# Kernel tuning notes

Measured on AMD Instinct MI355X. Metric: run time of the kernel, lower is better.

Reference implementation:

```python
import jax, jax.numpy as jnp
import numpy as np

N_NODES = 50000
N_EDGES = 500000
N_GRAPHS = 512


def _segmean(vals, ids, num):
    # avg aggregation: segment mean with safe divide for empty segments
    s = jax.ops.segment_sum(vals, ids, num_segments=num)
    c = jax.ops.segment_sum(jnp.ones((vals.shape[0], 1), vals.dtype), ids, num_segments=num)
    return s / jnp.maximum(c, 1.0)


def setup_inputs() -> dict:
    key = jax.random.key(0)
    ks = iter(jax.random.split(key, 64))

    def nrm(shape, scale=0.05):
        return jax.random.normal(next(ks), shape, dtype=jnp.float32) * scale

    inp = {}
    inp['x'] = nrm((N_NODES, 64), 1.0)
    inp['e'] = nrm((N_EDGES, 32), 1.0)
    inp['u'] = nrm((N_GRAPHS, 64), 1.0)
    inp['a'] = nrm((N_GRAPHS, 8), 1.0)
    inp['senders'] = jax.random.randint(next(ks), (N_EDGES,), 0, N_NODES)
    inp['receivers'] = jax.random.randint(next(ks), (N_EDGES,), 0, N_NODES)
    inp['node_graph'] = jnp.sort(jax.random.randint(next(ks), (N_NODES,), 0, N_GRAPHS))
    inp['edge_graph'] = jnp.sort(jax.random.randint(next(ks), (N_EDGES,), 0, N_GRAPHS))
    # block 1 (hidden 256)
    inp['We1'] = nrm((32, 256)); inp['be1'] = jnp.zeros((256,), jnp.float32)
    inp['Wn1'] = nrm((64, 256)); inp['Win1'] = nrm((256, 256)); inp['Wout1'] = nrm((256, 256)); inp['bn1'] = jnp.zeros((256,), jnp.float32)
    inp['Wg1'] = nrm((64, 256)); inp['Wgn1'] = nrm((256, 256)); inp['Wge1'] = nrm((256, 256)); inp['bg1'] = jnp.zeros((256,), jnp.float32)
    # block 2 (hidden 128)
    inp['We2'] = nrm((256, 128)); inp['be2'] = jnp.zeros((128,), jnp.float32)
    inp['Wn2'] = nrm((256, 128)); inp['Win2'] = nrm((128, 128)); inp['Wout2'] = nrm((128, 128)); inp['bn2'] = jnp.zeros((128,), jnp.float32)
    inp['Wg2'] = nrm((256, 128)); inp['Wgn2'] = nrm((128, 128)); inp['Wge2'] = nrm((128, 128)); inp['bg2'] = jnp.zeros((128,), jnp.float32)
    # global readout (global_features only)
    inp['Wga'] = nrm((128, 128)); inp['bga'] = jnp.zeros((128,), jnp.float32)
    # action-value MLP: (128 + 8) -> 256 -> 256 -> 1
    inp['Wa1'] = nrm((136, 256)); inp['ba1'] = jnp.zeros((256,), jnp.float32)
    inp['Wa2'] = nrm((256, 256)); inp['ba2'] = jnp.zeros((256,), jnp.float32)
    inp['Wa3'] = nrm((256, 1)); inp['ba3'] = jnp.zeros((1,), jnp.float32)
    return inp


def reference(x, e, u, a, senders, receivers, node_graph, edge_graph,
              We1, be1, Wn1, Win1, Wout1, bn1, Wg1, Wgn1, Wge1, bg1,
              We2, be2, Wn2, Win2, Wout2, bn2, Wg2, Wgn2, Wge2, bg2,
              Wga, bga, Wa1, ba1, Wa2, ba2, Wa3, ba3):
    # --- GraphNetwork block 1 (hidden 256) ---
    e1 = jax.nn.relu(e @ We1 + be1)                                  # [E,256]
    inc1 = _segmean(e1, receivers, N_NODES)                          # avg incoming per node
    out1 = _segmean(e1, senders, N_NODES)                            # avg outgoing per node
    n1 = jax.nn.relu(x @ Wn1 + inc1 @ Win1 + out1 @ Wout1 + bn1)     # [N,256]
    u1 = jax.nn.relu(u @ Wg1 + _segmean(n1, node_graph, N_GRAPHS) @ Wgn1
                     + _segmean(e1, edge_graph, N_GRAPHS) @ Wge1 + bg1)  # [B,256]
    # --- GraphNetwork block 2 (hidden 128) ---
    e2 = jax.nn.relu(e1 @ We2 + be2)                                 # [E,128]
    inc2 = _segmean(e2, receivers, N_NODES)
    out2 = _segmean(e2, senders, N_NODES)
    n2 = jax.nn.relu(n1 @ Wn2 + inc2 @ Win2 + out2 @ Wout2 + bn2)    # [N,128]
    u2 = jax.nn.relu(u1 @ Wg2 + _segmean(n2, node_graph, N_GRAPHS) @ Wgn2
                     + _segmean(e2, edge_graph, N_GRAPHS) @ Wge2 + bg2)  # [B,128]
    # --- global readout + action-value MLP ---
    state_value = u2 @ Wga + bga                                     # [B,128]
    h = jnp.concatenate([state_value, a], axis=1)                    # [B,136]
    h = jax.nn.relu(h @ Wa1 + ba1)
    h = jax.nn.relu(h @ Wa2 + ba2)
    return h @ Wa3 + ba3                                             # [B,1]
```

## Files before the change

kernel.cpp:

```cpp
#include <hip/hip_runtime.h>
#include <hip/hip_bf16.h>

#define N_NODES 50000
#define N_EDGES 500000
#define N_GRAPHS 512

#define FXS16 2048.0f
#define FXI16 4.8828125e-4f

__device__ __forceinline__ unsigned long long pk16x4(float4 v) {
    const unsigned long long a = (unsigned int)fmaf(v.x, FXS16, 0.5f);
    const unsigned long long b = (unsigned int)fmaf(v.y, FXS16, 0.5f);
    const unsigned long long c = (unsigned int)fmaf(v.z, FXS16, 0.5f);
    const unsigned long long d = (unsigned int)fmaf(v.w, FXS16, 0.5f);
    return a | (b << 16) | (c << 32) | (d << 48);
}

typedef __attribute__((ext_vector_type(8))) short bf16x8;
typedef __attribute__((ext_vector_type(4))) float f32x4;

__global__ __launch_bounds__(256) void prep_kernel(
    const float* __restrict__ We2,  const float* __restrict__ Wn1,
    const float* __restrict__ Win1, const float* __restrict__ Wout1,
    const float* __restrict__ Wn2,  const float* __restrict__ Win2,
    const float* __restrict__ Wout2,
    __hip_bfloat16* __restrict__ Wt2,  __hip_bfloat16* __restrict__ Wn1t,
    __hip_bfloat16* __restrict__ Win1t,__hip_bfloat16* __restrict__ Wout1t,
    __hip_bfloat16* __restrict__ Wn2t, __hip_bfloat16* __restrict__ Win2t,
    __hip_bfloat16* __restrict__ Wout2t)
{
    const int b = blockIdx.x, t = threadIdx.x;
    const float* src; __hip_bfloat16* dst; int K, N, base;
    if (b < 128)      { src = We2;   dst = Wt2;    K = 256; N = 128; base = 0; }
    else if (b < 192) { src = Wn1;   dst = Wn1t;   K = 64;  N = 256; base = 128; }
    else if (b < 448) { src = Win1;  dst = Win1t;  K = 256; N = 256; base = 192; }
    else if (b < 704) { src = Wout1; dst = Wout1t; K = 256; N = 256; base = 448; }
    else if (b < 832) { src = Wn2;   dst = Wn2t;   K = 256; N = 128; base = 704; }
    else if (b < 896) { src = Win2;  dst = Win2t;  K = 128; N = 128; base = 832; }
    else              { src = Wout2; dst = Wout2t; K = 128; N = 128; base = 896; }
    const int i = (b - base) * 256 + t;
    const int n = i / K, k = i - n * K;
    dst[i] = __float2bfloat16(src[(size_t)k * N + n]);
}


#define NTILES 196

__global__ __launch_bounds__(256) void count_kernel(
    const int* __restrict__ senders, const int* __restrict__ receivers,
    unsigned int* __restrict__ rc, unsigned int* __restrict__ sc)
{
    const int i = blockIdx.x * 256 + threadIdx.x;
    if (i < N_EDGES) {
        atomicAdd(&rc[receivers[i]], 1u);
        atomicAdd(&sc[senders[i]], 1u);
    }
}

__global__ __launch_bounds__(256) void scan_tile_sum(
    const unsigned int* __restrict__ rc, const unsigned int* __restrict__ sc,
    unsigned int* __restrict__ tsR, unsigned int* __restrict__ tsS)
{
    const int b = blockIdx.x;
    const int sel = (b >= NTILES);
    const int tile = sel ? b - NTILES : b;
    const unsigned int* src = sel ? sc : rc;
    unsigned int* ts = sel ? tsS : tsR;
    const int t = threadIdx.x;
    const int i = tile * 256 + t;
    unsigned int v = (i < N_NODES) ? src[i] : 0u;
    __shared__ unsigned int s[256];
    s[t] = v; __syncthreads();
    for (int off = 128; off > 0; off >>= 1) {
        if (t < off) s[t] += s[t + off];
        __syncthreads();
    }
    if (t == 0) ts[tile] = s[0];
}

__global__ __launch_bounds__(256) void scan_tile_offsets(
    unsigned int* __restrict__ tsR, unsigned int* __restrict__ tsS,
    int* __restrict__ roff, int* __restrict__ soff)
{
    __shared__ unsigned int s[256];
    const int t = threadIdx.x;
    for (int sel = 0; sel < 2; sel++) {
        unsigned int* ts = sel ? tsS : tsR;
        int* off = sel ? soff : roff;
        unsigned int v = (t < NTILES) ? ts[t] : 0u;
        s[t] = v; __syncthreads();
        for (int o = 1; o < 256; o <<= 1) {
            unsigned int x = (t >= o) ? s[t - o] : 0u;
            __syncthreads();
            s[t] += x;
            __syncthreads();
        }
        const unsigned int incl = s[t];
        if (t < NTILES) ts[t] = incl - v;
        if (t == NTILES - 1) off[N_NODES] = (int)incl;
        __syncthreads();
    }
}

__global__ __launch_bounds__(256) void scan_finalize(
    const unsigned int* __restrict__ rc, const unsigned int* __restrict__ sc,
    const unsigned int* __restrict__ tsR, const unsigned int* __restrict__ tsS,
    int* __restrict__ roff, int* __restrict__ soff,
    unsigned int* __restrict__ wpR, unsigned int* __restrict__ wpS)
{
    const int b = blockIdx.x;
    const int sel = (b >= NTILES);
    const int tile = sel ? b - NTILES : b;
    const unsigned int* src = sel ? sc : rc;
    const unsigned int* ts = sel ? tsS : tsR;
    int* off = sel ? soff : roff;
    unsigned int* wp = sel ? wpS : wpR;
    const int t = threadIdx.x, i = tile * 256 + t;
    unsigned int v = (i < N_NODES) ? src[i] : 0u;
    __shared__ unsigned int s[256];
    s[t] = v; __syncthreads();
    for (int o = 1; o < 256; o <<= 1) {
        unsigned int x = (t >= o) ? s[t - o] : 0u;
        __syncthreads();
        s[t] += x;
        __syncthreads();
    }
    const unsigned int excl = s[t] - v + ts[tile];
    if (i < N_NODES) { off[i] = (int)excl; wp[i] = excl; }
}

__global__ __launch_bounds__(256) void csr_fill(
    const int* __restrict__ senders, const int* __restrict__ receivers,
    unsigned int* __restrict__ wpR, unsigned int* __restrict__ wpS,
    int* __restrict__ csrR, int* __restrict__ csrS)
{
    const int i = blockIdx.x * 256 + threadIdx.x;
    if (i < N_EDGES) {
        csrR[atomicAdd(&wpR[receivers[i]], 1u)] = i;
        csrS[atomicAdd(&wpS[senders[i]], 1u)] = i;
    }
}

#define EPB 32
#define E1P 264
#define E2P 132

__global__ __launch_bounds__(256) void edge_kernel_csr(
    const float* __restrict__ e,
    const int* __restrict__ edge_graph,
    const float* __restrict__ We1, const float* __restrict__ be1,
    const __hip_bfloat16* __restrict__ Wt2,
    const float* __restrict__ be2,
    __hip_bfloat16* __restrict__ e1buf, unsigned short* __restrict__ e2buf,
    float* __restrict__ ge1, float* __restrict__ ge2, float* __restrict__ gecnt)
{
    __shared__ float eL[EPB * 32];
    __shared__ __hip_bfloat16 e1B[EPB * E1P];
    __shared__ float e2L[EPB * E2P];
    __shared__ int gidx[EPB];

    const int t = threadIdx.x;
    const long e0 = (long)blockIdx.x * EPB;

    for (int i = t; i < EPB * 32; i += 256) eL[i] = e[e0 * 32 + i];
    if (t < EPB) gidx[t] = edge_graph[e0 + t];
    __syncthreads();

    {
        const int c0 = (t & 63) * 4;
        const int jb = (t >> 6) * 8;
        float4 acc[8];
        const float4 b4 = *(const float4*)&be1[c0];
        #pragma unroll
        for (int j = 0; j < 8; j++) acc[j] = b4;
        for (int k = 0; k < 32; k += 4) {
            float4 v[8];
            #pragma unroll
            for (int j = 0; j < 8; j++) v[j] = *(const float4*)&eL[(jb + j) * 32 + k];
            #pragma unroll
            for (int kk = 0; kk < 4; kk++) {
                const float4 w = *(const float4*)&We1[(size_t)(k + kk) * 256 + c0];
                #pragma unroll
                for (int j = 0; j < 8; j++) {
                    const float vv = ((const float*)&v[j])[kk];
                    acc[j].x = fmaf(vv, w.x, acc[j].x);
                    acc[j].y = fmaf(vv, w.y, acc[j].y);
                    acc[j].z = fmaf(vv, w.z, acc[j].z);
                    acc[j].w = fmaf(vv, w.w, acc[j].w);
                }
            }
        }
        #pragma unroll
        for (int j = 0; j < 8; j++) {
            const float2 p0 = make_float2(fmaxf(acc[j].x, 0.f), fmaxf(acc[j].y, 0.f));
            const float2 p1 = make_float2(fmaxf(acc[j].z, 0.f), fmaxf(acc[j].w, 0.f));
            *(__hip_bfloat162*)&e1B[(jb + j) * E1P + c0]     = __float22bfloat162_rn(p0);
            *(__hip_bfloat162*)&e1B[(jb + j) * E1P + c0 + 2] = __float22bfloat162_rn(p1);
        }
    }
    __syncthreads();

    {
        const int wv = t >> 6, ln = t & 63;
        const int r0 = ln & 15, q = ln >> 4;
        f32x4 acc[2][2] = {{{0.f,0.f,0.f,0.f},{0.f,0.f,0.f,0.f}},
                           {{0.f,0.f,0.f,0.f},{0.f,0.f,0.f,0.f}}};
        const int n0 = (2 * wv) * 16 + r0;
        const int n1 = (2 * wv + 1) * 16 + r0;
        #pragma unroll
        for (int kb = 0; kb < 8; kb++) {
            const int k0 = kb * 32 + q * 8;
            const bf16x8 a0 = *(const bf16x8*)&e1B[(r0) * E1P + k0];
            const bf16x8 a1 = *(const bf16x8*)&e1B[(16 + r0) * E1P + k0];
            const bf16x8 b0 = *(const bf16x8*)&Wt2[(size_t)n0 * 256 + k0];
            const bf16x8 b1 = *(const bf16x8*)&Wt2[(size_t)n1 * 256 + k0];
            acc[0][0] = __builtin_amdgcn_mfma_f32_16x16x32_bf16(a0, b0, acc[0][0], 0, 0, 0);
            acc[0][1] = __builtin_amdgcn_mfma_f32_16x16x32_bf16(a0, b1, acc[0][1], 0, 0, 0);
            acc[1][0] = __builtin_amdgcn_mfma_f32_16x16x32_bf16(a1, b0, acc[1][0], 0, 0, 0);
            acc[1][1] = __builtin_amdgcn_mfma_f32_16x16x32_bf16(a1, b1, acc[1][1], 0, 0, 0);
        }
        const float bz0 = be2[2 * wv * 16 + r0];
        const float bz1 = be2[(2 * wv + 1) * 16 + r0];
        #pragma unroll
        for (int mt = 0; mt < 2; mt++) {
            const int m = mt * 16 + q * 4;
            #pragma unroll
            for (int r = 0; r < 4; r++) {
                e2L[(m + r) * E2P + 2 * wv * 16 + r0]       = fmaxf(acc[mt][0][r] + bz0, 0.f);
                e2L[(m + r) * E2P + (2 * wv + 1) * 16 + r0] = fmaxf(acc[mt][1][r] + bz1, 0.f);
            }
        }
    }
    __syncthreads();

    for (int i = t; i < EPB * 32; i += 256) {
        const int j = i >> 5, c8 = (i & 31) * 8;
        *(bf16x8*)&e1buf[(size_t)(e0 + j) * 256 + c8] = *(const bf16x8*)&e1B[j * E1P + c8];
    }
    for (int i = t; i < EPB * 32; i += 256) {
        const int j = i >> 5, c4 = (i & 31) * 4;
        const float4 v = *(const float4*)&e2L[j * E2P + c4];
        ushort4 pk;
        pk.x = (unsigned short)fmaf(v.x, FXS16, 0.5f);
        pk.y = (unsigned short)fmaf(v.y, FXS16, 0.5f);
        pk.z = (unsigned short)fmaf(v.z, FXS16, 0.5f);
        pk.w = (unsigned short)fmaf(v.w, FXS16, 0.5f);
        *(ushort4*)&e2buf[(size_t)(e0 + j) * 128 + c4] = pk;
    }

    if (gidx[0] == gidx[EPB - 1]) {
        const int g = gidx[0];
        float s = 0.f;
        #pragma unroll
        for (int j = 0; j < EPB; j++) s += __bfloat162float(e1B[j * E1P + t]);
        atomicAdd(&ge1[(size_t)g * 256 + t], s);
        if (t < 128) {
            float s2 = 0.f;
            #pragma unroll
            for (int j = 0; j < EPB; j++) s2 += e2L[j * E2P + t];
            atomicAdd(&ge2[(size_t)g * 128 + t], s2);
        }
        if (t == 0) atomicAdd(&gecnt[g], (float)EPB);
    } else {
        int j = 0;
        while (j < EPB) {
            const int g = gidx[j];
            int j2 = j;
            float s = 0.f;
            while (j2 < EPB && gidx[j2] == g) { s += __bfloat162float(e1B[j2 * E1P + t]); j2++; }
            atomicAdd(&ge1[(size_t)g * 256 + t], s);
            if (t < 128) {
                float s2 = 0.f;
                for (int jj = j; jj < j2; jj++) s2 += e2L[jj * E2P + t];
                atomicAdd(&ge2[(size_t)g * 128 + t], s2);
            }
            if (t == 0) atomicAdd(&gecnt[g], (float)(j2 - j));
            j = j2;
        }
    }
}

#define NPB 16
#define XP  72
#define K1P 264
#define K2P 136

__global__ __launch_bounds__(256) void node_kernel_csr(
    const float* __restrict__ x,
    const int* __restrict__ node_graph,
    const int* __restrict__ roff, const int* __restrict__ soff,
    const int* __restrict__ csrR, const int* __restrict__ csrS,
    const __hip_bfloat16* __restrict__ e1buf, const unsigned short* __restrict__ e2buf,
    const __hip_bfloat16* __restrict__ Wn1t, const __hip_bfloat16* __restrict__ Win1t,
    const __hip_bfloat16* __restrict__ Wout1t, const float* __restrict__ bn1,
    const __hip_bfloat16* __restrict__ Wn2t, const __hip_bfloat16* __restrict__ Win2t,
    const __hip_bfloat16* __restrict__ Wout2t, const float* __restrict__ bn2,
    float* __restrict__ gn1, float* __restrict__ gn2, float* __restrict__ gncnt)
{
    __shared__ __hip_bfloat16 xB[NPB * XP];
    __shared__ __hip_bfloat16 i1B[NPB * K1P];
    __shared__ __hip_bfloat16 o1B[NPB * K1P];
    __shared__ __hip_bfloat16 i2B[NPB * K2P];
    __shared__ __hip_bfloat16 o2B[NPB * K2P];
    __shared__ __hip_bfloat16 n1B[NPB * K1P];
    __shared__ __hip_bfloat16 n2B[NPB * K2P];
    __shared__ int gI[NPB];

    const int t = threadIdx.x;
    const long n0 = (long)blockIdx.x * NPB;

    if (t < NPB) gI[t] = node_graph[n0 + t];
    for (int i = t; i < NPB * 16; i += 256) {
        const int j = i >> 4, c4 = (i & 15) * 4;
        const float4 v = *(const float4*)&x[(n0 + j) * 64 + c4];
        *(__hip_bfloat162*)&xB[j * XP + c4]     = __float22bfloat162_rn(make_float2(v.x, v.y));
        *(__hip_bfloat162*)&xB[j * XP + c4 + 2] = __float22bfloat162_rn(make_float2(v.z, v.w));
    }

    const int wv = t >> 6, ln = t & 63;
    const int h = ln >> 5, l5 = ln & 31;
    const int* off = h ? soff : roff;
    const int* lst = h ? csrS : csrR;
    __hip_bfloat16* d1 = h ? o1B : i1B;
    __hip_bfloat16* d2 = h ? o2B : i2B;

    for (int jj = 0; jj < 4; jj++) {
        const int j = wv * 4 + jj;
        const long node = n0 + j;
        const int o = off[node], oE = off[node + 1];
        float a1[8] = {0.f,0.f,0.f,0.f,0.f,0.f,0.f,0.f};
        float a2[4] = {0.f,0.f,0.f,0.f};
        int i = o;
        int id = (i < oE) ? lst[i] : 0;
        while (i < oE) {
            const int idc = id;
            ++i;
            id = (i < oE) ? lst[i] : 0;
            const bf16x8 r1 = *(const bf16x8*)&e1buf[(size_t)idc * 256 + l5 * 8];
            const ushort4 r2 = *(const ushort4*)&e2buf[(size_t)idc * 128 + l5 * 4];
            #pragma unroll
            for (int c = 0; c < 8; c++)
                a1[c] += __uint_as_float(((unsigned int)(unsigned short)r1[c]) << 16);
            a2[0] += (float)r2.x; a2[1] += (float)r2.y;
            a2[2] += (float)r2.z; a2[3] += (float)r2.w;
        }
        const int cnt = oE - o;
        const float inv = 1.f / (float)(cnt > 0 ? cnt : 1);
        const float inv2 = inv * FXI16;
        #pragma unroll
        for (int c = 0; c < 4; c++) {
            *(__hip_bfloat162*)&d1[j * K1P + l5 * 8 + 2 * c] =
                __float22bfloat162_rn(make_float2(a1[2 * c] * inv, a1[2 * c + 1] * inv));
        }
        *(__hip_bfloat162*)&d2[j * K2P + l5 * 4] =
            __float22bfloat162_rn(make_float2(a2[0] * inv2, a2[1] * inv2));
        *(__hip_bfloat162*)&d2[j * K2P + l5 * 4 + 2] =
            __float22bfloat162_rn(make_float2(a2[2] * inv2, a2[3] * inv2));
    }
    __syncthreads();

    const int r0 = ln & 15, q = ln >> 4;

    {
        f32x4 acc[4] = {{0.f,0.f,0.f,0.f},{0.f,0.f,0.f,0.f},
                        {0.f,0.f,0.f,0.f},{0.f,0.f,0.f,0.f}};
        #pragma unroll
        for (int ks = 0; ks < 2; ks++) {
            const int k0 = ks * 32 + q * 8;
            const bf16x8 a = *(const bf16x8*)&xB[r0 * XP + k0];
            #pragma unroll
            for (int nn = 0; nn < 4; nn++) {
                const int n = (wv * 4 + nn) * 16 + r0;
                const bf16x8 b = *(const bf16x8*)&Wn1t[(size_t)n * 64 + k0];
                acc[nn] = __builtin_amdgcn_mfma_f32_16x16x32_bf16(a, b, acc[nn], 0, 0, 0);
            }
        }
        #pragma unroll
        for (int ks = 0; ks < 8; ks++) {
            const int k0 = ks * 32 + q * 8;
            const bf16x8 a = *(const bf16x8*)&i1B[r0 * K1P + k0];
            #pragma unroll
            for (int nn = 0; nn < 4; nn++) {
                const int n = (wv * 4 + nn) * 16 + r0;
                const bf16x8 b = *(const bf16x8*)&Win1t[(size_t)n * 256 + k0];
                acc[nn] = __builtin_amdgcn_mfma_f32_16x16x32_bf16(a, b, acc[nn], 0, 0, 0);
            }
        }
        #pragma unroll
        for (int ks = 0; ks < 8; ks++) {
            const int k0 = ks * 32 + q * 8;
            const bf16x8 a = *(const bf16x8*)&o1B[r0 * K1P + k0];
            #pragma unroll
            for (int nn = 0; nn < 4; nn++) {
                const int n = (wv * 4 + nn) * 16 + r0;
                const bf16x8 b = *(const bf16x8*)&Wout1t[(size_t)n * 256 + k0];
                acc[nn] = __builtin_amdgcn_mfma_f32_16x16x32_bf16(a, b, acc[nn], 0, 0, 0);
            }
        }
        #pragma unroll
        for (int nn = 0; nn < 4; nn++) {
            const int n = (wv * 4 + nn) * 16 + r0;
            const float bz = bn1[n];
            #pragma unroll
            for (int r = 0; r < 4; r++) {
                const int m = q * 4 + r;
                n1B[m * K1P + n] = __float2bfloat16(fmaxf(acc[nn][r] + bz, 0.f));
            }
        }
    }
    __syncthreads();

    if (gI[0] == gI[NPB - 1]) {
        float s = 0.f;
        #pragma unroll
        for (int j = 0; j < NPB; j++) s += __bfloat162float(n1B[j * K1P + t]);
        atomicAdd(&gn1[(size_t)gI[0] * 256 + t], s);
        if (t == 0) atomicAdd(&gncnt[gI[0]], (float)NPB);
    } else {
        int j = 0;
        while (j < NPB) {
            const int g = gI[j];
            int j2 = j;
            float s = 0.f;
            while (j2 < NPB && gI[j2] == g) { s += __bfloat162float(n1B[j2 * K1P + t]); j2++; }
            atomicAdd(&gn1[(size_t)g * 256 + t], s);
            if (t == 0) atomicAdd(&gncnt[g], (float)(j2 - j));
            j = j2;
        }
    }

    {
        f32x4 acc[2] = {{0.f,0.f,0.f,0.f},{0.f,0.f,0.f,0.f}};
        #pragma unroll
        for (int ks = 0; ks < 8; ks++) {
            const int k0 = ks * 32 + q * 8;
            const bf16x8 a = *(const bf16x8*)&n1B[r0 * K1P + k0];
            #pragma unroll
            for (int nn = 0; nn < 2; nn++) {
                const int n = (wv * 2 + nn) * 16 + r0;
                const bf16x8 b = *(const bf16x8*)&Wn2t[(size_t)n * 256 + k0];
                acc[nn] = __builtin_amdgcn_mfma_f32_16x16x32_bf16(a, b, acc[nn], 0, 0, 0);
            }
        }
        #pragma unroll
        for (int ks = 0; ks < 4; ks++) {
            const int k0 = ks * 32 + q * 8;
            const bf16x8 a = *(const bf16x8*)&i2B[r0 * K2P + k0];
            #pragma unroll
            for (int nn = 0; nn < 2; nn++) {
                const int n = (wv * 2 + nn) * 16 + r0;
                const bf16x8 b = *(const bf16x8*)&Win2t[(size_t)n * 128 + k0];
                acc[nn] = __builtin_amdgcn_mfma_f32_16x16x32_bf16(a, b, acc[nn], 0, 0, 0);
            }
        }
        #pragma unroll
        for (int ks = 0; ks < 4; ks++) {
            const int k0 = ks * 32 + q * 8;
            const bf16x8 a = *(const bf16x8*)&o2B[r0 * K2P + k0];
            #pragma unroll
            for (int nn = 0; nn < 2; nn++) {
                const int n = (wv * 2 + nn) * 16 + r0;
                const bf16x8 b = *(const bf16x8*)&Wout2t[(size_t)n * 128 + k0];
                acc[nn] = __builtin_amdgcn_mfma_f32_16x16x32_bf16(a, b, acc[nn], 0, 0, 0);
            }
        }
        #pragma unroll
        for (int nn = 0; nn < 2; nn++) {
            const int n = (wv * 2 + nn) * 16 + r0;
            const float bz = bn2[n];
            #pragma unroll
            for (int r = 0; r < 4; r++) {
                const int m = q * 4 + r;
                n2B[m * K2P + n] = __float2bfloat16(fmaxf(acc[nn][r] + bz, 0.f));
            }
        }
    }
    __syncthreads();

    if (t < 128) {
        if (gI[0] == gI[NPB - 1]) {
            float s = 0.f;
            #pragma unroll
            for (int j = 0; j < NPB; j++) s += __bfloat162float(n2B[j * K2P + t]);
            atomicAdd(&gn2[(size_t)gI[0] * 128 + t], s);
        } else {
            int j = 0;
            while (j < NPB) {
                const int g = gI[j];
                int j2 = j;
                float s = 0.f;
                while (j2 < NPB && gI[j2] == g) { s += __bfloat162float(n2B[j2 * K2P + t]); j2++; }
                atomicAdd(&gn2[(size_t)g * 128 + t], s);
                j = j2;
            }
        }
    }
}


__global__ __launch_bounds__(256) void edge_kernel(
    const float* __restrict__ e,
    const int* __restrict__ senders,
    const int* __restrict__ receivers,
    const int* __restrict__ edge_graph,
    const float* __restrict__ We1, const float* __restrict__ be1,
    const __hip_bfloat16* __restrict__ Wt2,
    const float* __restrict__ be2,
    unsigned long long* __restrict__ inc1u, unsigned long long* __restrict__ out1u,
    unsigned long long* __restrict__ inc2u, unsigned long long* __restrict__ out2u,
    float* __restrict__ rcnt, float* __restrict__ scnt,
    float* __restrict__ ge1, float* __restrict__ ge2, float* __restrict__ gecnt)
{
    __shared__ float eL[EPB * 32];
    __shared__ __hip_bfloat16 e1B[EPB * E1P];
    __shared__ float e2L[EPB * E2P];
    __shared__ int ridx[EPB], sidx[EPB], gidx[EPB];

    const int t = threadIdx.x;
    const long e0 = (long)blockIdx.x * EPB;

    for (int i = t; i < EPB * 32; i += 256) eL[i] = e[e0 * 32 + i];
    if (t < EPB) {
        ridx[t] = receivers[e0 + t];
        sidx[t] = senders[e0 + t];
        gidx[t] = edge_graph[e0 + t];
    }
    __syncthreads();

    {
        const int c0 = (t & 63) * 4;
        const int jb = (t >> 6) * 8;
        float4 acc[8];
        const float4 b4 = *(const float4*)&be1[c0];
        #pragma unroll
        for (int j = 0; j < 8; j++) acc[j] = b4;
        for (int k = 0; k < 32; k += 4) {
            float4 v[8];
            #pragma unroll
            for (int j = 0; j < 8; j++) v[j] = *(const float4*)&eL[(jb + j) * 32 + k];
            #pragma unroll
            for (int kk = 0; kk < 4; kk++) {
                const float4 w = *(const float4*)&We1[(size_t)(k + kk) * 256 + c0];
                #pragma unroll
                for (int j = 0; j < 8; j++) {
                    const float vv = ((const float*)&v[j])[kk];
                    acc[j].x = fmaf(vv, w.x, acc[j].x);
                    acc[j].y = fmaf(vv, w.y, acc[j].y);
                    acc[j].z = fmaf(vv, w.z, acc[j].z);
                    acc[j].w = fmaf(vv, w.w, acc[j].w);
                }
            }
        }
        #pragma unroll
        for (int j = 0; j < 8; j++) {
            const float2 p0 = make_float2(fmaxf(acc[j].x, 0.f), fmaxf(acc[j].y, 0.f));
            const float2 p1 = make_float2(fmaxf(acc[j].z, 0.f), fmaxf(acc[j].w, 0.f));
            *(__hip_bfloat162*)&e1B[(jb + j) * E1P + c0]     = __float22bfloat162_rn(p0);
            *(__hip_bfloat162*)&e1B[(jb + j) * E1P + c0 + 2] = __float22bfloat162_rn(p1);
        }
    }
    __syncthreads();

    {
        const int wv = t >> 6, ln = t & 63;
        const int r0 = ln & 15, q = ln >> 4;
        f32x4 acc[2][2] = {{{0.f,0.f,0.f,0.f},{0.f,0.f,0.f,0.f}},
                           {{0.f,0.f,0.f,0.f},{0.f,0.f,0.f,0.f}}};
        const int n0 = (2 * wv) * 16 + r0;
        const int n1 = (2 * wv + 1) * 16 + r0;
        #pragma unroll
        for (int kb = 0; kb < 8; kb++) {
            const int k0 = kb * 32 + q * 8;
            const bf16x8 a0 = *(const bf16x8*)&e1B[(r0) * E1P + k0];
            const bf16x8 a1 = *(const bf16x8*)&e1B[(16 + r0) * E1P + k0];
            const bf16x8 b0 = *(const bf16x8*)&Wt2[(size_t)n0 * 256 + k0];
            const bf16x8 b1 = *(const bf16x8*)&Wt2[(size_t)n1 * 256 + k0];
            acc[0][0] = __builtin_amdgcn_mfma_f32_16x16x32_bf16(a0, b0, acc[0][0], 0, 0, 0);
            acc[0][1] = __builtin_amdgcn_mfma_f32_16x16x32_bf16(a0, b1, acc[0][1], 0, 0, 0);
            acc[1][0] = __builtin_amdgcn_mfma_f32_16x16x32_bf16(a1, b0, acc[1][0], 0, 0, 0);
            acc[1][1] = __builtin_amdgcn_mfma_f32_16x16x32_bf16(a1, b1, acc[1][1], 0, 0, 0);
        }
        const float bz0 = be2[2 * wv * 16 + r0];
        const float bz1 = be2[(2 * wv + 1) * 16 + r0];
        #pragma unroll
        for (int mt = 0; mt < 2; mt++) {
            const int m = mt * 16 + q * 4;
            #pragma unroll
            for (int r = 0; r < 4; r++) {
                e2L[(m + r) * E2P + 2 * wv * 16 + r0]       = fmaxf(acc[mt][0][r] + bz0, 0.f);
                e2L[(m + r) * E2P + (2 * wv + 1) * 16 + r0] = fmaxf(acc[mt][1][r] + bz1, 0.f);
            }
        }
    }
    __syncthreads();

    {
        const int w = t & 63;
        const int ep = (t >> 6) & 1;
        unsigned long long* arr = (t < 128) ? inc1u : out1u;
        const int* idx = (t < 128) ? ridx : sidx;
        #pragma unroll
        for (int jj = 0; jj < EPB / 2; jj++) {
            const int j = jj * 2 + ep;
            const float2 v0 = __bfloat1622float2(*(const __hip_bfloat162*)&e1B[j * E1P + 4 * w]);
            const float2 v1 = __bfloat1622float2(*(const __hip_bfloat162*)&e1B[j * E1P + 4 * w + 2]);
            float4 v; v.x = v0.x; v.y = v0.y; v.z = v1.x; v.w = v1.y;
            atomicAdd(&arr[(size_t)idx[j] * 64 + w], pk16x4(v));
        }
    }
    {
        const int w = t & 31;
        const int eq = (t >> 5) & 3;
        unsigned long long* arr = (t < 128) ? inc2u : out2u;
        const int* idx = (t < 128) ? ridx : sidx;
        #pragma unroll
        for (int jj = 0; jj < EPB / 4; jj++) {
            const int j = jj * 4 + eq;
            const float4 v = *(const float4*)&e2L[j * E2P + 4 * w];
            atomicAdd(&arr[(size_t)idx[j] * 32 + w], pk16x4(v));
        }
    }
    if (gidx[0] == gidx[EPB - 1]) {
        const int g = gidx[0];
        float s = 0.f;
        #pragma unroll
        for (int j = 0; j < EPB; j++) s += __bfloat162float(e1B[j * E1P + t]);
        atomicAdd(&ge1[(size_t)g * 256 + t], s);
        if (t < 128) {
            float s2 = 0.f;
            #pragma unroll
            for (int j = 0; j < EPB; j++) s2 += e2L[j * E2P + t];
            atomicAdd(&ge2[(size_t)g * 128 + t], s2);
        }
        if (t == 0) atomicAdd(&gecnt[g], (float)EPB);
    } else {
        int j = 0;
        while (j < EPB) {
            const int g = gidx[j];
            int j2 = j;
            float s = 0.f;
            while (j2 < EPB && gidx[j2] == g) { s += __bfloat162float(e1B[j2 * E1P + t]); j2++; }
            atomicAdd(&ge1[(size_t)g * 256 + t], s);
            if (t < 128) {
                float s2 = 0.f;
                for (int jj = j; jj < j2; jj++) s2 += e2L[jj * E2P + t];
                atomicAdd(&ge2[(size_t)g * 128 + t], s2);
            }
            if (t == 0) atomicAdd(&gecnt[g], (float)(j2 - j));
            j = j2;
        }
    }
    if (t < EPB) {
        atomicAdd(&rcnt[ridx[t]], 1.f);
        atomicAdd(&scnt[sidx[t]], 1.f);
    }
}

__global__ __launch_bounds__(256) void node_kernel(
    const float* __restrict__ x,
    const int* __restrict__ node_graph,
    const unsigned long long* __restrict__ inc1u, const unsigned long long* __restrict__ out1u,
    const unsigned long long* __restrict__ inc2u, const unsigned long long* __restrict__ out2u,
    const float* __restrict__ rcnt, const float* __restrict__ scnt,
// ... 35 lines not shown
        const unsigned long long av = inc1u[n * 64 + w];
        const unsigned long long bv = out1u[n * 64 + w];
        const float rr = rrcp[j], sr = srcp[j];
        const float2 a01 = make_float2((float)(unsigned int)(av & 0xFFFF) * rr,
                                       (float)(unsigned int)((av >> 16) & 0xFFFF) * rr);
        const float2 a23 = make_float2((float)(unsigned int)((av >> 32) & 0xFFFF) * rr,
                                       (float)(unsigned int)(av >> 48) * rr);
        const float2 b01 = make_float2((float)(unsigned int)(bv & 0xFFFF) * sr,
                                       (float)(unsigned int)((bv >> 16) & 0xFFFF) * sr);
        const float2 b23 = make_float2((float)(unsigned int)((bv >> 32) & 0xFFFF) * sr,
                                       (float)(unsigned int)(bv >> 48) * sr);
        *(__hip_bfloat162*)&i1B[j * K1P + 4 * w]     = __float22bfloat162_rn(a01);
        *(__hip_bfloat162*)&i1B[j * K1P + 4 * w + 2] = __float22bfloat162_rn(a23);
        *(__hip_bfloat162*)&o1B[j * K1P + 4 * w]     = __float22bfloat162_rn(b01);
        *(__hip_bfloat162*)&o1B[j * K1P + 4 * w + 2] = __float22bfloat162_rn(b23);
    }
    for (int i = t; i < NPB * 32; i += 256) {
        const int j = i >> 5, w = i & 31;
        const size_t n = (size_t)(n0 + j);
        const unsigned long long av = inc2u[n * 32 + w];
        const unsigned long long bv = out2u[n * 32 + w];
        const float rr = rrcp[j], sr = srcp[j];
        const float2 a01 = make_float2((float)(unsigned int)(av & 0xFFFF) * rr,
                                       (float)(unsigned int)((av >> 16) & 0xFFFF) * rr);
        const float2 a23 = make_float2((float)(unsigned int)((av >> 32) & 0xFFFF) * rr,
                                       (float)(unsigned int)(av >> 48) * rr);
        const float2 b01 = make_float2((float)(unsigned int)(bv & 0xFFFF) * sr,
                                       (float)(unsigned int)((bv >> 16) & 0xFFFF) * sr);
        const float2 b23 = make_float2((float)(unsigned int)((bv >> 32) & 0xFFFF) * sr,
                                       (float)(unsigned int)(bv >> 48) * sr);
        *(__hip_bfloat162*)&i2B[j * K2P + 4 * w]     = __float22bfloat162_rn(a01);
        *(__hip_bfloat162*)&i2B[j * K2P + 4 * w + 2] = __float22bfloat162_rn(a23);
        *(__hip_bfloat162*)&o2B[j * K2P + 4 * w]     = __float22bfloat162_rn(b01);
        *(__hip_bfloat162*)&o2B[j * K2P + 4 * w + 2] = __float22bfloat162_rn(b23);
    }
    __syncthreads();

    const int wv = t >> 6, ln = t & 63;
    const int r0 = ln & 15, q = ln >> 4;

    {
        f32x4 acc[4] = {{0.f,0.f,0.f,0.f},{0.f,0.f,0.f,0.f},
                        {0.f,0.f,0.f,0.f},{0.f,0.f,0.f,0.f}};
        #pragma unroll
        for (int ks = 0; ks < 2; ks++) {
            const int k0 = ks * 32 + q * 8;
            const bf16x8 a = *(const bf16x8*)&xB[r0 * XP + k0];
            #pragma unroll
            for (int nn = 0; nn < 4; nn++) {
                const int n = (wv * 4 + nn) * 16 + r0;
                const bf16x8 b = *(const bf16x8*)&Wn1t[(size_t)n * 64 + k0];
                acc[nn] = __builtin_amdgcn_mfma_f32_16x16x32_bf16(a, b, acc[nn], 0, 0, 0);
            }
        }
        #pragma unroll
        for (int ks = 0; ks < 8; ks++) {
            const int k0 = ks * 32 + q * 8;
            const bf16x8 a = *(const bf16x8*)&i1B[r0 * K1P + k0];
            #pragma unroll
            for (int nn = 0; nn < 4; nn++) {
                const int n = (wv * 4 + nn) * 16 + r0;
                const bf16x8 b = *(const bf16x8*)&Win1t[(size_t)n * 256 + k0];
                acc[nn] = __builtin_amdgcn_mfma_f32_16x16x32_bf16(a, b, acc[nn], 0, 0, 0);
            }
        }
        #pragma unroll
        for (int ks = 0; ks < 8; ks++) {
            const int k0 = ks * 32 + q * 8;
            const bf16x8 a = *(const bf16x8*)&o1B[r0 * K1P + k0];
            #pragma unroll
            for (int nn = 0; nn < 4; nn++) {
                const int n = (wv * 4 + nn) * 16 + r0;
                const bf16x8 b = *(const bf16x8*)&Wout1t[(size_t)n * 256 + k0];
                acc[nn] = __builtin_amdgcn_mfma_f32_16x16x32_bf16(a, b, acc[nn], 0, 0, 0);
            }
        }
        #pragma unroll
        for (int nn = 0; nn < 4; nn++) {
            const int n = (wv * 4 + nn) * 16 + r0;
            const float bz = bn1[n];
            #pragma unroll
            for (int r = 0; r < 4; r++) {
                const int m = q * 4 + r;
                n1B[m * K1P + n] = __float2bfloat16(fmaxf(acc[nn][r] + bz, 0.f));
            }
        }
    }
    __syncthreads();

    if (gI[0] == gI[NPB - 1]) {
        float s = 0.f;
        #pragma unroll
        for (int j = 0; j < NPB; j++) s += __bfloat162float(n1B[j * K1P + t]);
        atomicAdd(&gn1[(size_t)gI[0] * 256 + t], s);
        if (t == 0) atomicAdd(&gncnt[gI[0]], (float)NPB);
    } else {
        int j = 0;
        while (j < NPB) {
            const int g = gI[j];
            int j2 = j;
            float s = 0.f;
            while (j2 < NPB && gI[j2] == g) { s += __bfloat162float(n1B[j2 * K1P + t]); j2++; }
            atomicAdd(&gn1[(size_t)g * 256 + t], s);
            if (t == 0) atomicAdd(&gncnt[g], (float)(j2 - j));
            j = j2;
        }
    }

    {
        f32x4 acc[2] = {{0.f,0.f,0.f,0.f},{0.f,0.f,0.f,0.f}};
        #pragma unroll
        for (int ks = 0; ks < 8; ks++) {
            const int k0 = ks * 32 + q * 8;
            const bf16x8 a = *(const bf16x8*)&n1B[r0 * K1P + k0];
            #pragma unroll
            for (int nn = 0; nn < 2; nn++) {
                const int n = (wv * 2 + nn) * 16 + r0;
                const bf16x8 b = *(const bf16x8*)&Wn2t[(size_t)n * 256 + k0];
                acc[nn] = __builtin_amdgcn_mfma_f32_16x16x32_bf16(a, b, acc[nn], 0, 0, 0);
            }
        }
        #pragma unroll
        for (int ks = 0; ks < 4; ks++) {
            const int k0 = ks * 32 + q * 8;
            const bf16x8 a = *(const bf16x8*)&i2B[r0 * K2P + k0];
            #pragma unroll
            for (int nn = 0; nn < 2; nn++) {
                const int n = (wv * 2 + nn) * 16 + r0;
                const bf16x8 b = *(const bf16x8*)&Win2t[(size_t)n * 128 + k0];
                acc[nn] = __builtin_amdgcn_mfma_f32_16x16x32_bf16(a, b, acc[nn], 0, 0, 0);
            }
        }
        #pragma unroll
        for (int ks = 0; ks < 4; ks++) {
            const int k0 = ks * 32 + q * 8;
            const bf16x8 a = *(const bf16x8*)&o2B[r0 * K2P + k0];
            #pragma unroll
            for (int nn = 0; nn < 2; nn++) {
                const int n = (wv * 2 + nn) * 16 + r0;
                const bf16x8 b = *(const bf16x8*)&Wout2t[(size_t)n * 128 + k0];
                acc[nn] = __builtin_amdgcn_mfma_f32_16x16x32_bf16(a, b, acc[nn], 0, 0, 0);
            }
        }
        #pragma unroll
        for (int nn = 0; nn < 2; nn++) {
            const int n = (wv * 2 + nn) * 16 + r0;
            const float bz = bn2[n];
            #pragma unroll
            for (int r = 0; r < 4; r++) {
                const int m = q * 4 + r;
                n2B[m * K2P + n] = __float2bfloat16(fmaxf(acc[nn][r] + bz, 0.f));
            }
        }
    }
    __syncthreads();

    if (t < 128) {
        if (gI[0] == gI[NPB - 1]) {
            float s = 0.f;
            #pragma unroll
            for (int j = 0; j < NPB; j++) s += __bfloat162float(n2B[j * K2P + t]);
            atomicAdd(&gn2[(size_t)gI[0] * 128 + t], s);
        } else {
            int j = 0;
            while (j < NPB) {
                const int g = gI[j];
                int j2 = j;
                float s = 0.f;
                while (j2 < NPB && gI[j2] == g) { s += __bfloat162float(n2B[j2 * K2P + t]); j2++; }
                atomicAdd(&gn2[(size_t)g * 128 + t], s);
                j = j2;
            }
        }
    }
}

__global__ __launch_bounds__(256) void graph_kernel(
    const float* __restrict__ u,
    const float* __restrict__ a,
    const float* __restrict__ ge1, const float* __restrict__ ge2,
    const float* __restrict__ gecnt,
    const float* __restrict__ gn1, const float* __restrict__ gn2,
    const float* __restrict__ gncnt,
    const float* __restrict__ Wg1, const float* __restrict__ Wgn1,
    const float* __restrict__ Wge1, const float* __restrict__ bg1,
    const float* __restrict__ Wg2, const float* __restrict__ Wgn2,
    const float* __restrict__ Wge2, const float* __restrict__ bg2,
    const float* __restrict__ Wga, const float* __restrict__ bga,
    const float* __restrict__ Wa1, const float* __restrict__ ba1,
    const float* __restrict__ Wa2, const float* __restrict__ ba2,
    const float* __restrict__ Wa3, const float* __restrict__ ba3,
    float* __restrict__ out)
{
    const int g = blockIdx.x;
    const int t = threadIdx.x;
    __shared__ float uL[64], mn1[256], me1[256], mn2[128], me2[128];
    __shared__ float u1L[256], u2L[128], hL[144], h1L[256], h2L[256];
    __shared__ float red[4];

    const float ec = 1.f / fmaxf(gecnt[g], 1.f);
    const float nc = 1.f / fmaxf(gncnt[g], 1.f);
    if (t < 64) uL[t] = u[(size_t)g * 64 + t];
    mn1[t] = gn1[(size_t)g * 256 + t] * nc;
    me1[t] = ge1[(size_t)g * 256 + t] * ec;
    if (t < 128) {
        mn2[t] = gn2[(size_t)g * 128 + t] * nc;
        me2[t] = ge2[(size_t)g * 128 + t] * ec;
    }
    if (t >= 136 && t < 144) hL[t] = 0.f;
    __syncthreads();

    {
        float acc = bg1[t];
        for (int k = 0; k < 64; k++)  acc = fmaf(uL[k],  Wg1[(size_t)k * 256 + t], acc);
        for (int k = 0; k < 256; k++) acc = fmaf(mn1[k], Wgn1[(size_t)k * 256 + t], acc);
        for (int k = 0; k < 256; k++) acc = fmaf(me1[k], Wge1[(size_t)k * 256 + t], acc);
        u1L[t] = fmaxf(acc, 0.f);
    }
    __syncthreads();
    if (t < 128) {
        float acc = bg2[t];
        for (int k = 0; k < 256; k++) acc = fmaf(u1L[k], Wg2[(size_t)k * 128 + t], acc);
        for (int k = 0; k < 128; k++) acc = fmaf(mn2[k], Wgn2[(size_t)k * 128 + t], acc);
        for (int k = 0; k < 128; k++) acc = fmaf(me2[k], Wge2[(size_t)k * 128 + t], acc);
        u2L[t] = fmaxf(acc, 0.f);
    }
    __syncthreads();
    if (t < 128) {
        float acc = bga[t];
        for (int k = 0; k < 128; k++) acc = fmaf(u2L[k], Wga[(size_t)k * 128 + t], acc);
        hL[t] = acc;
    }
    if (t >= 128 && t < 136) hL[t] = a[(size_t)g * 8 + (t - 128)];
    __syncthreads();
    {
        float acc = ba1[t];
        for (int k = 0; k < 136; k++) acc = fmaf(hL[k], Wa1[(size_t)k * 256 + t], acc);
        h1L[t] = fmaxf(acc, 0.f);
    }
    __syncthreads();
    {
        float acc = ba2[t];
        for (int k = 0; k < 256; k++) acc = fmaf(h1L[k], Wa2[(size_t)k * 256 + t], acc);
        h2L[t] = fmaxf(acc, 0.f);
    }
    __syncthreads();
    {
        float p = h2L[t] * Wa3[t];
        for (int off = 32; off > 0; off >>= 1) p += __shfl_down(p, off, 64);
        if ((t & 63) == 0) red[t >> 6] = p;
        __syncthreads();
        if (t == 0) out[g] = red[0] + red[1] + red[2] + red[3] + ba3[0];
    }
}

extern "C" void kernel_launch(void* const* d_in, const int* in_sizes, int n_in,
                              void* d_out, int out_size, void* d_ws, size_t ws_size,
                              hipStream_t stream) {
    const float* x          = (const float*)d_in[0];
    const float* e          = (const float*)d_in[1];
    const float* u          = (const float*)d_in[2];
    const float* a          = (const float*)d_in[3];
    const int*   senders    = (const int*)d_in[4];
    const int*   receivers  = (const int*)d_in[5];
    const int*   node_graph = (const int*)d_in[6];
    const int*   edge_graph = (const int*)d_in[7];
    const float* We1 = (const float*)d_in[8];  const float* be1 = (const float*)d_in[9];
    const float* Wn1 = (const float*)d_in[10]; const float* Win1 = (const float*)d_in[11];
    const float* Wout1 = (const float*)d_in[12]; const float* bn1 = (const float*)d_in[13];
    const float* Wg1 = (const float*)d_in[14]; const float* Wgn1 = (const float*)d_in[15];
    const float* Wge1 = (const float*)d_in[16]; const float* bg1 = (const float*)d_in[17];
    const float* We2 = (const float*)d_in[18]; const float* be2 = (const float*)d_in[19];
    const float* Wn2 = (const float*)d_in[20]; const float* Win2 = (const float*)d_in[21];
    const float* Wout2 = (const float*)d_in[22]; const float* bn2 = (const float*)d_in[23];
    const float* Wg2 = (const float*)d_in[24]; const float* Wgn2 = (const float*)d_in[25];
    const float* Wge2 = (const float*)d_in[26]; const float* bg2 = (const float*)d_in[27];
    const float* Wga = (const float*)d_in[28]; const float* bga = (const float*)d_in[29];
    const float* Wa1 = (const float*)d_in[30]; const float* ba1 = (const float*)d_in[31];
    const float* Wa2 = (const float*)d_in[32]; const float* ba2 = (const float*)d_in[33];
    const float* Wa3 = (const float*)d_in[34]; const float* ba3 = (const float*)d_in[35];

    {
        char* p = (char*)d_ws;
        auto take = [&p](size_t bytes) {
            char* q = p; p += (bytes + 15) & ~(size_t)15; return q;
        };
        unsigned int* rcntU = (unsigned int*)take((size_t)N_NODES * 4);
        unsigned int* scntU = (unsigned int*)take((size_t)N_NODES * 4);
        float* ge1   = (float*)take((size_t)N_GRAPHS * 256 * 4);
        float* ge2   = (float*)take((size_t)N_GRAPHS * 128 * 4);
        float* gecnt = (float*)take((size_t)N_GRAPHS * 4);
        float* gn1   = (float*)take((size_t)N_GRAPHS * 256 * 4);
        float* gn2   = (float*)take((size_t)N_GRAPHS * 128 * 4);
        float* gncnt = (float*)take((size_t)N_GRAPHS * 4);
        const size_t zero_bytes = (size_t)(p - (char*)d_ws);
        int* roff = (int*)take((size_t)(N_NODES + 1) * 4);
        int* soff = (int*)take((size_t)(N_NODES + 1) * 4);
        unsigned int* wpR = (unsigned int*)take((size_t)N_NODES * 4);
        unsigned int* wpS = (unsigned int*)take((size_t)N_NODES * 4);
        unsigned int* tsR = (unsigned int*)take(256 * 4);
        unsigned int* tsS = (unsigned int*)take(256 * 4);
        int* csrR = (int*)take((size_t)N_EDGES * 4);
        int* csrS = (int*)take((size_t)N_EDGES * 4);
        __hip_bfloat16* e1buf = (__hip_bfloat16*)take((size_t)N_EDGES * 256 * 2);
        unsigned short* e2buf = (unsigned short*)take((size_t)N_EDGES * 128 * 2);
        __hip_bfloat16* Wt2    = (__hip_bfloat16*)take((size_t)128 * 256 * 2);
        __hip_bfloat16* Wn1t   = (__hip_bfloat16*)take((size_t)256 * 64 * 2);
        __hip_bfloat16* Win1t  = (__hip_bfloat16*)take((size_t)256 * 256 * 2);
        __hip_bfloat16* Wout1t = (__hip_bfloat16*)take((size_t)256 * 256 * 2);
        __hip_bfloat16* Wn2t   = (__hip_bfloat16*)take((size_t)128 * 256 * 2);
        __hip_bfloat16* Win2t  = (__hip_bfloat16*)take((size_t)128 * 128 * 2);
        __hip_bfloat16* Wout2t = (__hip_bfloat16*)take((size_t)128 * 128 * 2);
        const size_t needed = (size_t)(p - (char*)d_ws);

        if (ws_size >= needed) {
            hipMemsetAsync(d_ws, 0, zero_bytes, stream);

            prep_kernel<<<960, 256, 0, stream>>>(
                We2, Wn1, Win1, Wout1, Wn2, Win2, Wout2,
                Wt2, Wn1t, Win1t, Wout1t, Wn2t, Win2t, Wout2t);

            count_kernel<<<(N_EDGES + 255) / 256, 256, 0, stream>>>(
                senders, receivers, rcntU, scntU);
            scan_tile_sum<<<2 * NTILES, 256, 0, stream>>>(rcntU, scntU, tsR, tsS);
            scan_tile_offsets<<<1, 256, 0, stream>>>(tsR, tsS, roff, soff);
            scan_finalize<<<2 * NTILES, 256, 0, stream>>>(
                rcntU, scntU, tsR, tsS, roff, soff, wpR, wpS);
            csr_fill<<<(N_EDGES + 255) / 256, 256, 0, stream>>>(
                senders, receivers, wpR, wpS, csrR, csrS);

            edge_kernel_csr<<<N_EDGES / EPB, 256, 0, stream>>>(
                e, edge_graph, We1, be1, Wt2, be2,
                e1buf, e2buf, ge1, ge2, gecnt);

            node_kernel_csr<<<N_NODES / NPB, 256, 0, stream>>>(
                x, node_graph, roff, soff, csrR, csrS, e1buf, e2buf,
                Wn1t, Win1t, Wout1t, bn1, Wn2t, Win2t, Wout2t, bn2,
                gn1, gn2, gncnt);

            graph_kernel<<<N_GRAPHS, 256, 0, stream>>>(
                u, a, ge1, ge2, gecnt, gn1, gn2, gncnt,
                Wg1, Wgn1, Wge1, bg1, Wg2, Wgn2, Wge2, bg2,
                Wga, bga, Wa1, ba1, Wa2, ba2, Wa3, ba3, (float*)d_out);
            return;
        }
    }

    unsigned long long* uw = (unsigned long long*)d_ws;
    unsigned long long* inc1u = uw;                       uw += (size_t)N_NODES * 64;
    unsigned long long* out1u = uw;                       uw += (size_t)N_NODES * 64;
    unsigned long long* inc2u = uw;                       uw += (size_t)N_NODES * 32;
    unsigned long long* out2u = uw;                       uw += (size_t)N_NODES * 32;
    float* fw = (float*)uw;
    float* rcnt = fw;  fw += N_NODES;
    float* scnt = fw;  fw += N_NODES;
    float* ge1  = fw;  fw += (size_t)N_GRAPHS * 256;
    float* ge2  = fw;  fw += (size_t)N_GRAPHS * 128;
    float* gecnt = fw; fw += N_GRAPHS;
    float* gn1  = fw;  fw += (size_t)N_GRAPHS * 256;
    float* gn2  = fw;  fw += (size_t)N_GRAPHS * 128;
    float* gncnt = fw; fw += N_GRAPHS;
    const size_t total_bytes = (char*)fw - (char*)d_ws;
    __hip_bfloat16* bw = (__hip_bfloat16*)fw;
    __hip_bfloat16* Wt2    = bw;  bw += 128 * 256;
    __hip_bfloat16* Wn1t   = bw;  bw += 256 * 64;
    __hip_bfloat16* Win1t  = bw;  bw += 256 * 256;
    __hip_bfloat16* Wout1t = bw;  bw += 256 * 256;
    __hip_bfloat16* Wn2t   = bw;  bw += 128 * 256;
    __hip_bfloat16* Win2t  = bw;  bw += 128 * 128;
    __hip_bfloat16* Wout2t = bw;  bw += 128 * 128;

    hipMemsetAsync(d_ws, 0, total_bytes, stream);

    prep_kernel<<<960, 256, 0, stream>>>(
        We2, Wn1, Win1, Wout1, Wn2, Win2, Wout2,
        Wt2, Wn1t, Win1t, Wout1t, Wn2t, Win2t, Wout2t);

    edge_kernel<<<N_EDGES / EPB, 256, 0, stream>>>(
        e, senders, receivers, edge_graph, We1, be1, Wt2, be2,
        inc1u, out1u, inc2u, out2u, rcnt, scnt, ge1, ge2, gecnt);

    node_kernel<<<N_NODES / NPB, 256, 0, stream>>>(
        x, node_graph, inc1u, out1u, inc2u, out2u, rcnt, scnt,
        Wn1t, Win1t, Wout1t, bn1, Wn2t, Win2t, Wout2t, bn2, gn1, gn2, gncnt);

    graph_kernel<<<N_GRAPHS, 256, 0, stream>>>(
        u, a, ge1, ge2, gecnt, gn1, gn2, gncnt,
        Wg1, Wgn1, Wge1, bg1, Wg2, Wgn2, Wge2, bg2,
        Wga, bga, Wa1, ba1, Wa2, ba2, Wa3, ba3, (float*)d_out);
}
```

Baseline: 1.043 ms.

## Split edge features into L2-sized column slices gathered by separate mean kernels

Instead of writing full e1 (256 bf16) and e2 (fixed-point) rows per edge and gathering them inside the node kernel, the edge work is split into three 128-column slices (e2, then e1 halves). Each slice is written to a single 128-wide buffer and aggregated by a dedicated CSR gather-mean kernel into dense per-node incoming and outgoing arrays. The aim is to keep the gathered working set small enough to stay cache-resident during random gathers. In exchange it recomputes the e1 projection twice, adds extra launches and dense per-node buffers, and switches e2 storage from 16-bit fixed point to bf16.

```diff
diff --git a/kernel.cpp b/kernel.cpp
--- a/kernel.cpp
+++ b/kernel.cpp
@@ -18,6 +18,10 @@
 
 typedef __attribute__((ext_vector_type(8))) short bf16x8;
 typedef __attribute__((ext_vector_type(4))) float f32x4;
+
+__device__ __forceinline__ float bf16u_to_f(unsigned short u) {
+    return __uint_as_float(((unsigned int)u) << 16);
+}
 
 __global__ __launch_bounds__(256) void prep_kernel(
     const float* __restrict__ We2,  const float* __restrict__ Wn1,
@@ -145,13 +149,13 @@
 #define E1P 264
 #define E2P 132
 
-__global__ __launch_bounds__(256) void edge_kernel_csr(
+__global__ __launch_bounds__(256) void edge_kernel_e2(
     const float* __restrict__ e,
     const int* __restrict__ edge_graph,
     const float* __restrict__ We1, const float* __restrict__ be1,
     const __hip_bfloat16* __restrict__ Wt2,
     const float* __restrict__ be2,
-    __hip_bfloat16* __restrict__ e1buf, unsigned short* __restrict__ e2buf,
+    __hip_bfloat16* __restrict__ bufA,
     float* __restrict__ ge1, float* __restrict__ ge2, float* __restrict__ gecnt)
 {
     __shared__ float eL[EPB * 32];
@@ -234,18 +238,11 @@
     __syncthreads();
 
     for (int i = t; i < EPB * 32; i += 256) {
-        const int j = i >> 5, c8 = (i & 31) * 8;
-        *(bf16x8*)&e1buf[(size_t)(e0 + j) * 256 + c8] = *(const bf16x8*)&e1B[j * E1P + c8];
-    }
-    for (int i = t; i < EPB * 32; i += 256) {
         const int j = i >> 5, c4 = (i & 31) * 4;
         const float4 v = *(const float4*)&e2L[j * E2P + c4];
-        ushort4 pk;
-        pk.x = (unsigned short)fmaf(v.x, FXS16, 0.5f);
-        pk.y = (unsigned short)fmaf(v.y, FXS16, 0.5f);
-        pk.z = (unsigned short)fmaf(v.z, FXS16, 0.5f);
-        pk.w = (unsigned short)fmaf(v.w, FXS16, 0.5f);
-        *(ushort4*)&e2buf[(size_t)(e0 + j) * 128 + c4] = pk;
+        __hip_bfloat16* d = &bufA[(size_t)(e0 + j) * 128 + c4];
+        *(__hip_bfloat162*)&d[0] = __float22bfloat162_rn(make_float2(v.x, v.y));
+        *(__hip_bfloat162*)&d[2] = __float22bfloat162_rn(make_float2(v.z, v.w));
     }
 
     if (gidx[0] == gidx[EPB - 1]) {
@@ -280,17 +277,98 @@
     }
 }
 
+__global__ __launch_bounds__(256) void edge_half_kernel(
+    const float* __restrict__ e,
+    const float* __restrict__ We1, const float* __restrict__ be1,
+    const int c_base,
+    __hip_bfloat16* __restrict__ bufA)
+{
+    __shared__ float eL[EPB * 32];
+    const int t = threadIdx.x;
+    const long e0 = (long)blockIdx.x * EPB;
+    for (int i = t; i < EPB * 32; i += 256) eL[i] = e[e0 * 32 + i];
+    __syncthreads();
+
+    const int c0 = (t & 31) * 4;
+    const int jb = (t >> 5) * 4;
+    float4 acc[4];
+    const float4 b4 = *(const float4*)&be1[c_base + c0];
+    #pragma unroll
+    for (int j = 0; j < 4; j++) acc[j] = b4;
+    for (int k = 0; k < 32; k += 4) {
+        float4 v[4];
+        #pragma unroll
+        for (int j = 0; j < 4; j++) v[j] = *(const float4*)&eL[(jb + j) * 32 + k];
+        #pragma unroll
+        for (int kk = 0; kk < 4; kk++) {
+            const float4 w = *(const float4*)&We1[(size_t)(k + kk) * 256 + c_base + c0];
+            #pragma unroll
+            for (int j = 0; j < 4; j++) {
+                const float vv = ((const float*)&v[j])[kk];
+                acc[j].x = fmaf(vv, w.x, acc[j].x);
+                acc[j].y = fmaf(vv, w.y, acc[j].y);
+                acc[j].z = fmaf(vv, w.z, acc[j].z);
+                acc[j].w = fmaf(vv, w.w, acc[j].w);
+            }
+        }
+    }
+    #pragma unroll
+    for (int j = 0; j < 4; j++) {
+        const float2 p0 = make_float2(fmaxf(acc[j].x, 0.f), fmaxf(acc[j].y, 0.f));
+        const float2 p1 = make_float2(fmaxf(acc[j].z, 0.f), fmaxf(acc[j].w, 0.f));
+        __hip_bfloat16* d = &bufA[(size_t)(e0 + jb + j) * 128 + c0];
+        *(__hip_bfloat162*)&d[0] = __float22bfloat162_rn(p0);
+        *(__hip_bfloat162*)&d[2] = __float22bfloat162_rn(p1);
+    }
+}
+
+__global__ __launch_bounds__(256) void gather_mean_kernel(
+    const __hip_bfloat16* __restrict__ bufA,
+    const int* __restrict__ roff, const int* __restrict__ soff,
+    const int* __restrict__ csrR, const int* __restrict__ csrS,
+    __hip_bfloat16* __restrict__ dstR, __hip_bfloat16* __restrict__ dstS,
+    const int dst_stride, const int col0)
+{
+    const int t = threadIdx.x;
+    const int hw = t >> 5, l5 = t & 31;
+    const long task = (long)blockIdx.x * 8 + hw;
+    if (task >= 2L * N_NODES) return;
+    const int node = (int)(task >> 1), side = (int)(task & 1);
+    const int* off = side ? soff : roff;
+    const int* lst = side ? csrS : csrR;
+    __hip_bfloat16* dst = side ? dstS : dstR;
+
+    const int o = off[node], oE = off[node + 1];
+    float a0 = 0.f, a1 = 0.f, a2 = 0.f, a3 = 0.f;
+    int i = o;
+    int id = (i < oE) ? lst[i] : 0;
+    while (i < oE) {
+        const int idc = id;
+        ++i;
+        id = (i < oE) ? lst[i] : 0;
+        const ushort4 r = *(const ushort4*)&bufA[(size_t)idc * 128 + l5 * 4];
+        a0 += bf16u_to_f(r.x);
+        a1 += bf16u_to_f(r.y);
+        a2 += bf16u_to_f(r.z);
+        a3 += bf16u_to_f(r.w);
+    }
+    const int cnt = oE - o;
+    const float inv = 1.f / (float)(cnt > 0 ? cnt : 1);
+    __hip_bfloat16* d = &dst[(size_t)node * dst_stride + col0 + l5 * 4];
+    *(__hip_bfloat162*)&d[0] = __float22bfloat162_rn(make_float2(a0 * inv, a1 * inv));
+    *(__hip_bfloat162*)&d[2] = __float22bfloat162_rn(make_float2(a2 * inv, a3 * inv));
+}
+
 #define NPB 16
 #define XP  72
 #define K1P 264
 #define K2P 136
 
-__global__ __launch_bounds__(256) void node_kernel_csr(
+__global__ __launch_bounds__(256) void node_kernel_dense(
     const float* __restrict__ x,
     const int* __restrict__ node_graph,
-    const int* __restrict__ roff, const int* __restrict__ soff,
-    const int* __restrict__ csrR, const int* __restrict__ csrS,
-    const __hip_bfloat16* __restrict__ e1buf, const unsigned short* __restrict__ e2buf,
+    const __hip_bfloat16* __restrict__ i1d, const __hip_bfloat16* __restrict__ o1d,
+    const __hip_bfloat16* __restrict__ i2d, const __hip_bfloat16* __restrict__ o2d,
     const __hip_bfloat16* __restrict__ Wn1t, const __hip_bfloat16* __restrict__ Win1t,
     const __hip_bfloat16* __restrict__ Wout1t, const float* __restrict__ bn1,
     const __hip_bfloat16* __restrict__ Wn2t, const __hip_bfloat16* __restrict__ Win2t,
@@ -316,49 +394,19 @@
         *(__hip_bfloat162*)&xB[j * XP + c4]     = __float22bfloat162_rn(make_float2(v.x, v.y));
         *(__hip_bfloat162*)&xB[j * XP + c4 + 2] = __float22bfloat162_rn(make_float2(v.z, v.w));
     }
+    for (int i = t; i < NPB * 32; i += 256) {
+        const int j = i >> 5, c8 = (i & 31) * 8;
+        *(bf16x8*)&i1B[j * K1P + c8] = *(const bf16x8*)&i1d[(size_t)(n0 + j) * 256 + c8];
+        *(bf16x8*)&o1B[j * K1P + c8] = *(const bf16x8*)&o1d[(size_t)(n0 + j) * 256 + c8];
+    }
+    for (int i = t; i < NPB * 16; i += 256) {
+        const int j = i >> 4, c8 = (i & 15) * 8;
+        *(bf16x8*)&i2B[j * K2P + c8] = *(const bf16x8*)&i2d[(size_t)(n0 + j) * 128 + c8];
+        *(bf16x8*)&o2B[j * K2P + c8] = *(const bf16x8*)&o2d[(size_t)(n0 + j) * 128 + c8];
+    }
+    __syncthreads();
 
     const int wv = t >> 6, ln = t & 63;
-    const int h = ln >> 5, l5 = ln & 31;
-    const int* off = h ? soff : roff;
-    const int* lst = h ? csrS : csrR;
-    __hip_bfloat16* d1 = h ? o1B : i1B;
-    __hip_bfloat16* d2 = h ? o2B : i2B;
-
-    for (int jj = 0; jj < 4; jj++) {
-        const int j = wv * 4 + jj;
-        const long node = n0 + j;
-        const int o = off[node], oE = off[node + 1];
-        float a1[8] = {0.f,0.f,0.f,0.f,0.f,0.f,0.f,0.f};
-        float a2[4] = {0.f,0.f,0.f,0.f};
-        int i = o;
-        int id = (i < oE) ? lst[i] : 0;
-        while (i < oE) {
-            const int idc = id;
-            ++i;
-            id = (i < oE) ? lst[i] : 0;
-            const bf16x8 r1 = *(const bf16x8*)&e1buf[(size_t)idc * 256 + l5 * 8];
-            const ushort4 r2 = *(const ushort4*)&e2buf[(size_t)idc * 128 + l5 * 4];
-            #pragma unroll
-            for (int c = 0; c < 8; c++)
-                a1[c] += __uint_as_float(((unsigned int)(unsigned short)r1[c]) << 16);
-            a2[0] += (float)r2.x; a2[1] += (float)r2.y;
-            a2[2] += (float)r2.z; a2[3] += (float)r2.w;
-        }
-        const int cnt = oE - o;
-        const float inv = 1.f / (float)(cnt > 0 ? cnt : 1);
-        const float inv2 = inv * FXI16;
-        #pragma unroll
-        for (int c = 0; c < 4; c++) {
-            *(__hip_bfloat162*)&d1[j * K1P + l5 * 8 + 2 * c] =
-                __float22bfloat162_rn(make_float2(a1[2 * c] * inv, a1[2 * c + 1] * inv));
-        }
-        *(__hip_bfloat162*)&d2[j * K2P + l5 * 4] =
-            __float22bfloat162_rn(make_float2(a2[0] * inv2, a2[1] * inv2));
-        *(__hip_bfloat162*)&d2[j * K2P + l5 * 4 + 2] =
-            __float22bfloat162_rn(make_float2(a2[2] * inv2, a2[3] * inv2));
-    }
-    __syncthreads();
-
     const int r0 = ln & 15, q = ln >> 4;
 
     {
@@ -1000,8 +1048,11 @@
         unsigned int* tsS = (unsigned int*)take(256 * 4);
         int* csrR = (int*)take((size_t)N_EDGES * 4);
         int* csrS = (int*)take((size_t)N_EDGES * 4);
-        __hip_bfloat16* e1buf = (__hip_bfloat16*)take((size_t)N_EDGES * 256 * 2);
-        unsigned short* e2buf = (unsigned short*)take((size_t)N_EDGES * 128 * 2);
+        __hip_bfloat16* i1d = (__hip_bfloat16*)take((size_t)N_NODES * 256 * 2);
+        __hip_bfloat16* o1d = (__hip_bfloat16*)take((size_t)N_NODES * 256 * 2);
+        __hip_bfloat16* i2d = (__hip_bfloat16*)take((size_t)N_NODES * 128 * 2);
+        __hip_bfloat16* o2d = (__hip_bfloat16*)take((size_t)N_NODES * 128 * 2);
+        __hip_bfloat16* bufA = (__hip_bfloat16*)take((size_t)N_EDGES * 128 * 2);
         __hip_bfloat16* Wt2    = (__hip_bfloat16*)take((size_t)128 * 256 * 2);
         __hip_bfloat16* Wn1t   = (__hip_bfloat16*)take((size_t)256 * 64 * 2);
         __hip_bfloat16* Win1t  = (__hip_bfloat16*)take((size_t)256 * 256 * 2);
@@ -1027,12 +1078,21 @@
             csr_fill<<<(N_EDGES + 255) / 256, 256, 0, stream>>>(
                 senders, receivers, wpR, wpS, csrR, csrS);
 
-            edge_kernel_csr<<<N_EDGES / EPB, 256, 0, stream>>>(
-                e, edge_graph, We1, be1, Wt2, be2,
-                e1buf, e2buf, ge1, ge2, gecnt);
-
-            node_kernel_csr<<<N_NODES / NPB, 256, 0, stream>>>(
-                x, node_graph, roff, soff, csrR, csrS, e1buf, e2buf,
+            edge_kernel_e2<<<N_EDGES / EPB, 256, 0, stream>>>(
+                e, edge_graph, We1, be1, Wt2, be2, bufA, ge1, ge2, gecnt);
+            gather_mean_kernel<<<(2 * N_NODES + 7) / 8, 256, 0, stream>>>(
+                bufA, roff, soff, csrR, csrS, i2d, o2d, 128, 0);
+
+            edge_half_kernel<<<N_EDGES / EPB, 256, 0, stream>>>(e, We1, be1, 0, bufA);
+            gather_mean_kernel<<<(2 * N_NODES + 7) / 8, 256, 0, stream>>>(
+                bufA, roff, soff, csrR, csrS, i1d, o1d, 256, 0);
+
+            edge_half_kernel<<<N_EDGES / EPB, 256, 0, stream>>>(e, We1, be1, 128, bufA);
+            gather_mean_kernel<<<(2 * N_NODES + 7) / 8, 256, 0, stream>>>(
+                bufA, roff, soff, csrR, csrS, i1d, o1d, 256, 128);
+
+            node_kernel_dense<<<N_NODES / NPB, 256, 0, stream>>>(
+                x, node_graph, i1d, o1d, i2d, o2d,
                 Wn1t, Win1t, Wout1t, bn1, Wn2t, Win2t, Wout2t, bn2,
                 gn1, gn2, gncnt);
 
```

Measured after the change: 1.129 ms. +8.2%, slower.
